# Kernel tuning notes

Hardware: AMD Instinct MI355X
Metric: run time of the kernel (lower is better)

Reference implementation:

```python
import jax, jax.numpy as jnp
import numpy as np
import math


def setup_inputs() -> dict:
    key = jax.random.key(0)
    k1, k2 = jax.random.split(key)
    q = jax.random.normal(k1, (2, 8, 2048, 64), dtype=jnp.float32)
    v = jax.random.normal(k2, (2, 8, 2048, 64), dtype=jnp.float32)
    return {"q": q, "v": v}


def reference(q, v):
    # q, v: [B, H, L, D]. Softmax-free Gaussian-kernel attention.
    # squared L2 distance via expanded form: ||qi||^2 + ||qj||^2 - 2 qi.qj
    # (same math as the original's broadcasted difference, without the
    #  O(B,H,L,L,D) intermediate)
    d = q.shape[-1]
    sq = jnp.sum(q * q, axis=-1)                      # [B, H, L]
    dots = jnp.einsum('bhid,bhjd->bhij', q, q)        # [B, H, L, L]
    sq_l2 = sq[..., :, None] + sq[..., None, :] - 2.0 * dots
    score = jnp.exp(-1.0 / (2.0 * math.sqrt(d)) * sq_l2)  # [B, H, L, L]
    return jnp.einsum('bhij,bhjd->bhid', score, v)    # [B, H, L, D]
```

## Files before the change

### kernel.cpp

```cpp
#include <hip/hip_runtime.h>
#include <hip/hip_bf16.h>
#include <stdint.h>

typedef __bf16 bf16_t;
typedef bf16_t bf16x4 __attribute__((ext_vector_type(4)));
typedef bf16_t bf16x8 __attribute__((ext_vector_type(8)));
typedef float f32x16 __attribute__((ext_vector_type(16)));
typedef float fvec4 __attribute__((ext_vector_type(4)));
typedef unsigned int u32x4v __attribute__((ext_vector_type(4)));

#define LEN 2048
#define DIM 64
#define NH  16

#define C_L8  0.18033688011112043f
#define C_L16 0.09016844005556021f

__device__ __forceinline__ float fexp2(float x) {
  float r;
  asm("v_exp_f32 %0, %1\n\ts_nop 0" : "=v"(r) : "v"(x));
  return r;
}

__device__ __forceinline__ unsigned pk2(float lo, float hi) {
  union { bf16_t h; unsigned short u; } a, b;
  a.h = (bf16_t)lo; b.h = (bf16_t)hi;
  return (unsigned)a.u | ((unsigned)b.u << 16);
}

__device__ __forceinline__ void glds16(const void* g, void* l) {
  __builtin_amdgcn_global_load_lds(
      (const __attribute__((address_space(1))) void*)g,
      (__attribute__((address_space(3))) void*)l, 16, 0, 0);
}

__device__ __forceinline__ int swk(int row, int b) {
  return row * 128 + (b ^ ((row & 7) << 4));
}
__device__ __forceinline__ int swv(int row, int b) {
  return row * 256 + (b ^ ((row & 7) << 4));
}

__global__ __launch_bounds__(256) void prepass(
    const float* __restrict__ q, const float* __restrict__ v,
    bf16_t* __restrict__ kb, bf16_t* __restrict__ vt, float* __restrict__ sqw) {
  __shared__ float wlds[64];
  const int b = blockIdx.x;
  const int h = b >> 5, jb = b & 31;
  const int t = threadIdx.x;
  const float* qh = q + ((size_t)h * LEN + jb * 64) * DIM;
  const float* vh = v + ((size_t)h * LEN + jb * 64) * DIM;

  const int dl = t & 15, jg = t >> 4;
  const int d0 = dl * 4, j0 = jg * 4;
  fvec4 r0 = *(const fvec4*)(vh + (j0 + 0) * DIM + d0);
  fvec4 r1 = *(const fvec4*)(vh + (j0 + 1) * DIM + d0);
  fvec4 r2 = *(const fvec4*)(vh + (j0 + 2) * DIM + d0);
  fvec4 r3 = *(const fvec4*)(vh + (j0 + 3) * DIM + d0);

  {
    const int j = t >> 2, kd0 = (t & 3) * 16;
    const float* qp = qh + j * DIM + kd0;
    fvec4 x0 = *(const fvec4*)(qp);
    fvec4 x1 = *(const fvec4*)(qp + 4);
    fvec4 x2 = *(const fvec4*)(qp + 8);
    fvec4 x3 = *(const fvec4*)(qp + 12);
    float s = 0.f;
    bf16x8 o0, o1;
#pragma unroll
    for (int e = 0; e < 4; ++e) {
      bf16_t h0 = (bf16_t)x0[e]; o0[e]     = h0; float f0 = (float)h0; s += f0 * f0;
      bf16_t h1 = (bf16_t)x1[e]; o0[e + 4] = h1; float f1 = (float)h1; s += f1 * f1;
      bf16_t h2 = (bf16_t)x2[e]; o1[e]     = h2; float f2 = (float)h2; s += f2 * f2;
      bf16_t h3 = (bf16_t)x3[e]; o1[e + 4] = h3; float f3 = (float)h3; s += f3 * f3;
    }
    bf16_t* kp = kb + ((size_t)h * LEN + jb * 64 + j) * DIM + kd0;
    *(bf16x8*)kp = o0;
    *(bf16x8*)(kp + 8) = o1;
    s += __shfl_xor(s, 1);
    s += __shfl_xor(s, 2);
    if ((t & 3) == 0) {
      wlds[j] = fexp2(-s * C_L16);
      sqw[h * LEN + jb * 64 + j] = s * C_L16;
    }
  }
  __syncthreads();

  {
    const float w0 = wlds[j0], w1 = wlds[j0 + 1], w2 = wlds[j0 + 2], w3 = wlds[j0 + 3];
#pragma unroll
    for (int dd = 0; dd < 4; ++dd) {
      bf16x4 o;
      o[0] = (bf16_t)(r0[dd] * w0);
      o[1] = (bf16_t)(r1[dd] * w1);
      o[2] = (bf16_t)(r2[dd] * w2);
      o[3] = (bf16_t)(r3[dd] * w3);
      *(bf16x4*)(vt + ((size_t)h * DIM + d0 + dd) * LEN + jb * 64 + j0) = o;
    }
  }
}

__global__ __launch_bounds__(512, 2) void soft_attn_main(
    const bf16_t* __restrict__ kb, const bf16_t* __restrict__ vt,
    const float* __restrict__ sqw, float* __restrict__ out) {
  __shared__ __align__(16) char smem[98304];

  const int tid  = threadIdx.x;
  const int lane = tid & 63;
  const int wave = tid >> 6;
  const int rg   = wave & 1;
  const int par  = wave >> 1;
  const int g    = lane >> 5;
  const int nn   = lane & 31;

  const int b  = blockIdx.x;
  const int wg = ((b & 7) << 5) | (b >> 3);
  const int bh = wg >> 4;
  const int qb = wg & 15;

  const bf16_t* kh  = kb + (size_t)bh * LEN * DIM;
  const bf16_t* vth = vt + (size_t)bh * DIM * LEN;

  const int qrow0 = qb * 128 + rg * 64 + nn;
  bf16x8 qf0[4], qf1[4];
  {
    const bf16_t* qp0 = kh + (size_t)qrow0 * DIM;
    const bf16_t* qp1 = kh + (size_t)(qrow0 + 32) * DIM;
#pragma unroll
    for (int kc = 0; kc < 4; ++kc) {
      qf0[kc] = *(const bf16x8*)(qp0 + kc * 16 + g * 8);
      qf1[kc] = *(const bf16x8*)(qp1 + kc * 16 + g * 8);
    }
  }
  const float hq0 = sqw[bh * LEN + qrow0];
  const float hq1 = sqw[bh * LEN + qrow0 + 32];

  const bf16_t* ksrc[2];
  const bf16_t* vsrc[2];
#pragma unroll
  for (int s = 0; s < 2; ++s) {
    const int krow = wave * 16 + s * 8 + (lane >> 3);
    const int kby  = ((lane & 7) * 16) ^ ((lane >> 3) << 4);
    ksrc[s] = kh + (size_t)krow * DIM + (kby >> 1);
    const int vrow = wave * 8 + s * 4 + (lane >> 4);
    const int vby  = ((lane & 15) * 16) ^ ((vrow & 7) << 4);
    vsrc[s] = vth + (size_t)vrow * LEN + (vby >> 1);
  }
  char* kdst = smem + wave * 2048;
  char* vdst = smem + 49152 + wave * 2048;

  f32x16 acc00 = {}, acc01 = {}, acc10 = {}, acc11 = {};

#pragma unroll
  for (int s = 0; s < 2; ++s) {
    glds16(ksrc[s], kdst + s * 1024);
    glds16(vsrc[s], vdst + s * 1024);
  }
#pragma unroll
  for (int s = 0; s < 2; ++s) {
    glds16(ksrc[s] + (size_t)128 * DIM, kdst + 16384 + s * 1024);
    glds16(vsrc[s] + (size_t)128,       vdst + 16384 + s * 1024);
  }

  int bufo = 0;
  for (int it = 0; it < 16; ++it) {
    if (it < 15) {
      asm volatile("s_waitcnt vmcnt(4)" ::: "memory");
    } else {
      asm volatile("s_waitcnt vmcnt(0)" ::: "memory");
    }
    __builtin_amdgcn_sched_barrier(0);
    __builtin_amdgcn_s_barrier();
    __builtin_amdgcn_sched_barrier(0);

    const char* kb0 = smem + bufo;
    const char* vb0 = smem + 49152 + bufo;

    bf16x8 kf0 = *(const bf16x8*)(kb0 + swk(par * 32 + nn, 0 * 32 + g * 16));
    bf16x8 kf1 = *(const bf16x8*)(kb0 + swk(par * 32 + nn, 1 * 32 + g * 16));
    bf16x8 kf2 = *(const bf16x8*)(kb0 + swk(par * 32 + nn, 2 * 32 + g * 16));
    bf16x8 kf3 = *(const bf16x8*)(kb0 + swk(par * 32 + nn, 3 * 32 + g * 16));
    f32x16 t0 = {}, t1 = {};
    __builtin_amdgcn_s_setprio(1);
    t0 = __builtin_amdgcn_mfma_f32_32x32x16_bf16(kf0, qf0[0], t0, 0, 0, 0);
    t1 = __builtin_amdgcn_mfma_f32_32x32x16_bf16(kf0, qf1[0], t1, 0, 0, 0);
    t0 = __builtin_amdgcn_mfma_f32_32x32x16_bf16(kf1, qf0[1], t0, 0, 0, 0);
    t1 = __builtin_amdgcn_mfma_f32_32x32x16_bf16(kf1, qf1[1], t1, 0, 0, 0);
    t0 = __builtin_amdgcn_mfma_f32_32x32x16_bf16(kf2, qf0[2], t0, 0, 0, 0);
    t1 = __builtin_amdgcn_mfma_f32_32x32x16_bf16(kf2, qf1[2], t1, 0, 0, 0);
    t0 = __builtin_amdgcn_mfma_f32_32x32x16_bf16(kf3, qf0[3], t0, 0, 0, 0);
    t1 = __builtin_amdgcn_mfma_f32_32x32x16_bf16(kf3, qf1[3], t1, 0, 0, 0);
    __builtin_amdgcn_s_setprio(0);

    bf16x8 af00, af01, af10, af11;
    {
      unsigned P[8];
#pragma unroll
      for (int e = 0; e < 8; ++e) {
        float s0 = fexp2(__builtin_fmaf(t0[2 * e],     C_L8, -hq0));
        float s1 = fexp2(__builtin_fmaf(t0[2 * e + 1], C_L8, -hq0));
        P[e] = pk2(s0, s1);
      }
      asm volatile("v_permlane32_swap_b32 %0, %1" : "+v"(P[0]), "+v"(P[2]));
      asm volatile("v_permlane32_swap_b32 %0, %1" : "+v"(P[1]), "+v"(P[3]));
      asm volatile("v_permlane32_swap_b32 %0, %1" : "+v"(P[4]), "+v"(P[6]));
      asm volatile("v_permlane32_swap_b32 %0, %1" : "+v"(P[5]), "+v"(P[7]));
      u32x4v f0v = { P[0], P[1], P[2], P[3] };
      u32x4v f1v = { P[4], P[5], P[6], P[7] };
      af00 = __builtin_bit_cast(bf16x8, f0v);
      af01 = __builtin_bit_cast(bf16x8, f1v);
    }
    {
      unsigned P[8];
#pragma unroll
      for (int e = 0; e < 8; ++e) {
        float s0 = fexp2(__builtin_fmaf(t1[2 * e],     C_L8, -hq1));
        float s1 = fexp2(__builtin_fmaf(t1[2 * e + 1], C_L8, -hq1));
        P[e] = pk2(s0, s1);
      }
      asm volatile("v_permlane32_swap_b32 %0, %1" : "+v"(P[0]), "+v"(P[2]));
      asm volatile("v_permlane32_swap_b32 %0, %1" : "+v"(P[1]), "+v"(P[3]));
      asm volatile("v_permlane32_swap_b32 %0, %1" : "+v"(P[4]), "+v"(P[6]));
      asm volatile("v_permlane32_swap_b32 %0, %1" : "+v"(P[5]), "+v"(P[7]));
      u32x4v f0v = { P[0], P[1], P[2], P[3] };
      u32x4v f1v = { P[4], P[5], P[6], P[7] };
      af10 = __builtin_bit_cast(bf16x8, f0v);
      af11 = __builtin_bit_cast(bf16x8, f1v);
    }

    {
      bf16x8 v0 = *(const bf16x8*)(vb0 + swv(nn,      par * 64 + g * 16));
      bf16x8 v1 = *(const bf16x8*)(vb0 + swv(32 + nn, par * 64 + g * 16));
      bf16x8 v2 = *(const bf16x8*)(vb0 + swv(nn,      par * 64 + 32 + g * 16));
      bf16x8 v3 = *(const bf16x8*)(vb0 + swv(32 + nn, par * 64 + 32 + g * 16));
      __builtin_amdgcn_s_setprio(1);
      acc00 = __builtin_amdgcn_mfma_f32_32x32x16_bf16(af00, v0, acc00, 0, 0, 0);
      acc01 = __builtin_amdgcn_mfma_f32_32x32x16_bf16(af00, v1, acc01, 0, 0, 0);
      acc10 = __builtin_amdgcn_mfma_f32_32x32x16_bf16(af10, v0, acc10, 0, 0, 0);
      acc11 = __builtin_amdgcn_mfma_f32_32x32x16_bf16(af10, v1, acc11, 0, 0, 0);
      acc00 = __builtin_amdgcn_mfma_f32_32x32x16_bf16(af01, v2, acc00, 0, 0, 0);
      acc01 = __builtin_amdgcn_mfma_f32_32x32x16_bf16(af01, v3, acc01, 0, 0, 0);
      acc10 = __builtin_amdgcn_mfma_f32_32x32x16_bf16(af11, v2, acc10, 0, 0, 0);
      acc11 = __builtin_amdgcn_mfma_f32_32x32x16_bf16(af11, v3, acc11, 0, 0, 0);
      __builtin_amdgcn_s_setprio(0);
    }

    if (it + 2 < 16) {
      int nbo = bufo + 32768; if (nbo >= 49152) nbo -= 49152;
#pragma unroll
      for (int s = 0; s < 2; ++s) {
        glds16(ksrc[s] + (size_t)(it + 2) * 128 * DIM, kdst + nbo + s * 1024);
        glds16(vsrc[s] + (size_t)(it + 2) * 128,       vdst + nbo + s * 1024);
      }
    }

    bufo += 16384; if (bufo >= 49152) bufo = 0;
  }

  __syncthreads();
  float* xb = (float*)smem;
  if (par != 0) {
    const int slot = (par - 1) * 4 + rg * 2;
    float* d0 = xb + slot * 2048;
    float* d1 = xb + (slot + 1) * 2048;
#pragma unroll
    for (int r = 0; r < 16; ++r) {
      d0[r * 64 + lane]        = acc00[r];
      d0[1024 + r * 64 + lane] = acc01[r];
      d1[r * 64 + lane]        = acc10[r];
      d1[1024 + r * 64 + lane] = acc11[r];
    }
  }
  __syncthreads();
  if (par == 0) {
    float* op = out + ((size_t)bh * LEN + qb * 128 + rg * 64) * DIM;
#pragma unroll
    for (int r = 0; r < 16; ++r) {
      const int row = (r & 3) + 8 * (r >> 2) + 4 * g;
      float a00 = acc00[r], a01 = acc01[r], a10 = acc10[r], a11 = acc11[r];
#pragma unroll
      for (int p = 1; p < 4; ++p) {
        const int slot = (p - 1) * 4 + rg * 2;
        const float* s0 = xb + slot * 2048;
        const float* s1 = xb + (slot + 1) * 2048;
        a00 += s0[r * 64 + lane];
        a01 += s0[1024 + r * 64 + lane];
        a10 += s1[r * 64 + lane];
        a11 += s1[1024 + r * 64 + lane];
      }
      op[(size_t)row * DIM + nn]               = a00;
      op[(size_t)row * DIM + 32 + nn]          = a01;
      op[(size_t)(32 + row) * DIM + nn]        = a10;
      op[(size_t)(32 + row) * DIM + 32 + nn]   = a11;
    }
  }
}

__device__ __forceinline__ int swfb(int row, int byte) {
  return row * 128 + (byte ^ ((row & 7) << 4));
}

__global__ __launch_bounds__(512, 2) void soft_attn_fb(
    const float* __restrict__ q, const float* __restrict__ v,
    float* __restrict__ out) {
  __shared__ __align__(16) char smem[33280];
  const int tid = threadIdx.x;
  const int lane = tid & 63;
  const int wave = tid >> 6;
  const int rg = wave & 3;
  const int parity = wave >> 2;
  const int tp = tid & 255;
  const int g = lane >> 5;
  const int nn = lane & 31;
  const int wg = ((blockIdx.x & 7) << 5) | (blockIdx.x >> 3);
  const int bh = wg >> 4;
  const int qb = wg & 15;
  const float* qh = q + (size_t)bh * LEN * DIM;
  const float* vh = v + (size_t)bh * LEN * DIM;
  char* kbufp = smem + parity * 8192;
  char* vbufp = smem + 16384 + parity * 8192;
  float* wkp = (float*)(smem + 32768) + parity * 64;
  const int qrow = qb * 128 + rg * 32 + nn;
  bf16x8 qf[4];
  float sq = 0.f;
  {
    const float* qp = qh + (size_t)qrow * DIM;
#pragma unroll
    for (int kc = 0; kc < 4; ++kc) {
      const int d0 = kc * 16 + g * 8;
      fvec4 x = *(const fvec4*)(qp + d0);
      fvec4 y = *(const fvec4*)(qp + d0 + 4);
      bf16x8 t;
#pragma unroll
      for (int e = 0; e < 4; ++e) {
        bf16_t h0 = (bf16_t)x[e]; t[e] = h0; float f0 = (float)h0; sq += f0 * f0;
        bf16_t h1 = (bf16_t)y[e]; t[e + 4] = h1; float f1 = (float)h1; sq += f1 * f1;
      }
      qf[kc] = t;
    }
  }
  sq += __shfl_xor(sq, 32);
  const float hq = sq * C_L16;
  f32x16 acc0 = {};
  f32x16 acc1 = {};
  for (int it = 0; it < 16; ++it) {
    const int jt = it * 2 + parity;
    const float* kg = qh + (size_t)jt * 64 * DIM;
    const float* vg = vh + (size_t)jt * 64 * DIM;
    __syncthreads();
#pragma unroll
    for (int s = 0; s < 2; ++s) {
      const int c = tp + 256 * s;
      const int j = c >> 3;
      const int d0 = (c & 7) * 8;
      fvec4 x = *(const fvec4*)(kg + j * DIM + d0);
      fvec4 y = *(const fvec4*)(kg + j * DIM + d0 + 4);
      bf16x8 t; float p = 0.f;
#pragma unroll
      for (int e = 0; e < 4; ++e) {
        bf16_t h0 = (bf16_t)x[e]; t[e] = h0; float f0 = (float)h0; p += f0 * f0;
        bf16_t h1 = (bf16_t)y[e]; t[e + 4] = h1; float f1 = (float)h1; p += f1 * f1;
      }
      *(bf16x8*)(kbufp + swfb(j, d0 * 2)) = t;
      p += __shfl_xor(p, 1);
      p += __shfl_xor(p, 2);
      p += __shfl_xor(p, 4);
      if ((lane & 7) == 0) wkp[j] = fexp2(-p * C_L16);
    }
    __syncthreads();
    float vl[2][8];
    const int vd = tp & 63;
    const int vw = tp >> 6;
#pragma unroll
    for (int s = 0; s < 2; ++s) {
      const int j0 = vw * 8 + 32 * s;
      const float* vp = vg + j0 * DIM + vd;
#pragma unroll
      for (int r = 0; r < 8; ++r) vl[s][r] = vp[r * DIM];
    }
    bf16x8 af[4];
#pragma unroll
    for (int jsub = 0; jsub < 2; ++jsub) {
      f32x16 t = {};
#pragma unroll
      for (int kc = 0; kc < 4; ++kc) {
        bf16x8 kf = *(const bf16x8*)(kbufp + swfb(jsub * 32 + nn, kc * 32 + g * 16));
        t = __builtin_amdgcn_mfma_f32_32x32x16_bf16(kf, qf[kc], t, 0, 0, 0);
      }
      unsigned P[8];
#pragma unroll
      for (int e = 0; e < 8; ++e) {
        float s0 = fexp2(__builtin_fmaf(t[2 * e], C_L8, -hq));
        float s1 = fexp2(__builtin_fmaf(t[2 * e + 1], C_L8, -hq));
        P[e] = pk2(s0, s1);
      }
      asm volatile("v_permlane32_swap_b32 %0, %1" : "+v"(P[0]), "+v"(P[2]));
      asm volatile("v_permlane32_swap_b32 %0, %1" : "+v"(P[1]), "+v"(P[3]));
      asm volatile("v_permlane32_swap_b32 %0, %1" : "+v"(P[4]), "+v"(P[6]));
      asm volatile("v_permlane32_swap_b32 %0, %1" : "+v"(P[5]), "+v"(P[7]));
      u32x4v f0v = { P[0], P[1], P[2], P[3] };
      u32x4v f1v = { P[4], P[5], P[6], P[7] };
      af[jsub * 2] = __builtin_bit_cast(bf16x8, f0v);
      af[jsub * 2 + 1] = __builtin_bit_cast(bf16x8, f1v);
    }
#pragma unroll
    for (int s = 0; s < 2; ++s) {
      const int j0 = vw * 8 + 32 * s;
      bf16x8 t;
#pragma unroll
      for (int r = 0; r < 8; ++r) {
        float w = wkp[j0 + r];
        t[r] = (bf16_t)(vl[s][r] * w);
      }
      *(bf16x8*)(vbufp + swfb(vd, j0 * 2)) = t;
    }
    __syncthreads();
#pragma unroll
    for (int kc = 0; kc < 4; ++kc) {
      bf16x8 v0 = *(const bf16x8*)(vbufp + swfb(nn, kc * 32 + g * 16));
      bf16x8 v1 = *(const bf16x8*)(vbufp + swfb(32 + nn, kc * 32 + g * 16));
      acc0 = __builtin_amdgcn_mfma_f32_32x32x16_bf16(af[kc], v0, acc0, 0, 0, 0);
      acc1 = __builtin_amdgcn_mfma_f32_32x32x16_bf16(af[kc], v1, acc1, 0, 0, 0);
    }
  }
  __syncthreads();
  float* xb = (float*)smem + rg * 2048;
  if (parity == 1) {
#pragma unroll
    for (int r = 0; r < 16; ++r) {
      xb[r * 64 + lane] = acc0[r];
      xb[(16 + r) * 64 + lane] = acc1[r];
    }
  }
  __syncthreads();
  if (parity == 0) {
    float* op = out + ((size_t)bh * LEN + qb * 128 + rg * 32) * DIM;
#pragma unroll
    for (int r = 0; r < 16; ++r) {
      const int row = (r & 3) + 8 * (r >> 2) + 4 * g;
      op[(size_t)row * DIM + nn] = acc0[r] + xb[r * 64 + lane];
      op[(size_t)row * DIM + 32 + nn] = acc1[r] + xb[(16 + r) * 64 + lane];
    }
  }
}

extern "C" void kernel_launch(void* const* d_in, const int* in_sizes, int n_in,
                              void* d_out, int out_size, void* d_ws, size_t ws_size,
                              hipStream_t stream) {
  const float* q = (const float*)d_in[0];
  const float* v = (const float*)d_in[1];
  float* out = (float*)d_out;
  (void)in_sizes; (void)n_in; (void)out_size;

  const size_t KB_BYTES = (size_t)NH * LEN * DIM * 2;
  const size_t NEED = KB_BYTES * 2 + (size_t)NH * LEN * 4;
  if (ws_size >= NEED) {
    bf16_t* kb  = (bf16_t*)d_ws;
    bf16_t* vt  = (bf16_t*)((char*)d_ws + KB_BYTES);
    float*  sqw = (float*)((char*)d_ws + KB_BYTES * 2);
    prepass<<<dim3(512), dim3(256), 0, stream>>>(q, v, kb, vt, sqw);
    soft_attn_main<<<dim3(256), dim3(512), 0, stream>>>(kb, vt, sqw, out);
  } else {
    soft_attn_fb<<<dim3(256), dim3(512), 0, stream>>>(q, v, out);
  }
}
```

Measured before the change: 96.72 us.

## Fuse bf16 prepass into main kernel via cooperative grid sync

```diff
diff --git a/kernel.cpp b/kernel.cpp
--- a/kernel.cpp
+++ b/kernel.cpp
@@ -1,6 +1,9 @@
 #include <hip/hip_runtime.h>
 #include <hip/hip_bf16.h>
+#include <hip/hip_cooperative_groups.h>
 #include <stdint.h>
+
+namespace cg = cooperative_groups;
 
 typedef __bf16 bf16_t;
 typedef bf16_t bf16x4 __attribute__((ext_vector_type(4)));
@@ -41,69 +44,12 @@
   return row * 256 + (b ^ ((row & 7) << 4));
 }
 
-__global__ __launch_bounds__(256) void prepass(
+__global__ __launch_bounds__(512, 2) void soft_attn_coop(
     const float* __restrict__ q, const float* __restrict__ v,
-    bf16_t* __restrict__ kb, bf16_t* __restrict__ vt, float* __restrict__ sqw) {
-  __shared__ float wlds[64];
-  const int b = blockIdx.x;
-  const int h = b >> 5, jb = b & 31;
-  const int t = threadIdx.x;
-  const float* qh = q + ((size_t)h * LEN + jb * 64) * DIM;
-  const float* vh = v + ((size_t)h * LEN + jb * 64) * DIM;
-
-  const int dl = t & 15, jg = t >> 4;
-  const int d0 = dl * 4, j0 = jg * 4;
-  fvec4 r0 = *(const fvec4*)(vh + (j0 + 0) * DIM + d0);
-  fvec4 r1 = *(const fvec4*)(vh + (j0 + 1) * DIM + d0);
-  fvec4 r2 = *(const fvec4*)(vh + (j0 + 2) * DIM + d0);
-  fvec4 r3 = *(const fvec4*)(vh + (j0 + 3) * DIM + d0);
-
-  {
-    const int j = t >> 2, kd0 = (t & 3) * 16;
-    const float* qp = qh + j * DIM + kd0;
-    fvec4 x0 = *(const fvec4*)(qp);
-    fvec4 x1 = *(const fvec4*)(qp + 4);
-    fvec4 x2 = *(const fvec4*)(qp + 8);
-    fvec4 x3 = *(const fvec4*)(qp + 12);
-    float s = 0.f;
-    bf16x8 o0, o1;
-#pragma unroll
-    for (int e = 0; e < 4; ++e) {
-      bf16_t h0 = (bf16_t)x0[e]; o0[e]     = h0; float f0 = (float)h0; s += f0 * f0;
-      bf16_t h1 = (bf16_t)x1[e]; o0[e + 4] = h1; float f1 = (float)h1; s += f1 * f1;
-      bf16_t h2 = (bf16_t)x2[e]; o1[e]     = h2; float f2 = (float)h2; s += f2 * f2;
-      bf16_t h3 = (bf16_t)x3[e]; o1[e + 4] = h3; float f3 = (float)h3; s += f3 * f3;
-    }
-    bf16_t* kp = kb + ((size_t)h * LEN + jb * 64 + j) * DIM + kd0;
-    *(bf16x8*)kp = o0;
-    *(bf16x8*)(kp + 8) = o1;
-    s += __shfl_xor(s, 1);
-    s += __shfl_xor(s, 2);
-    if ((t & 3) == 0) {
-      wlds[j] = fexp2(-s * C_L16);
-      sqw[h * LEN + jb * 64 + j] = s * C_L16;
-    }
-  }
-  __syncthreads();
-
-  {
-    const float w0 = wlds[j0], w1 = wlds[j0 + 1], w2 = wlds[j0 + 2], w3 = wlds[j0 + 3];
-#pragma unroll
-    for (int dd = 0; dd < 4; ++dd) {
-      bf16x4 o;
-      o[0] = (bf16_t)(r0[dd] * w0);
-      o[1] = (bf16_t)(r1[dd] * w1);
-      o[2] = (bf16_t)(r2[dd] * w2);
-      o[3] = (bf16_t)(r3[dd] * w3);
-      *(bf16x4*)(vt + ((size_t)h * DIM + d0 + dd) * LEN + jb * 64 + j0) = o;
-    }
-  }
-}
-
-__global__ __launch_bounds__(512, 2) void soft_attn_main(
-    const bf16_t* __restrict__ kb, const bf16_t* __restrict__ vt,
-    const float* __restrict__ sqw, float* __restrict__ out) {
+    bf16_t* __restrict__ kb, bf16_t* __restrict__ vt,
+    float* __restrict__ out) {
   __shared__ __align__(16) char smem[98304];
+  __shared__ float s_lds[128];
 
   const int tid  = threadIdx.x;
   const int lane = tid & 63;
@@ -118,22 +64,92 @@
   const int bh = wg >> 4;
   const int qb = wg & 15;
 
-  const bf16_t* kh  = kb + (size_t)bh * LEN * DIM;
-  const bf16_t* vth = vt + (size_t)bh * DIM * LEN;
+  const float* qh = q + (size_t)bh * LEN * DIM;
+  const float* vh = v + (size_t)bh * LEN * DIM;
+  bf16_t* khw  = kb + (size_t)bh * LEN * DIM;
+  bf16_t* vthw = vt + (size_t)bh * DIM * LEN;
+
+  const int dl = tid & 15, jg = tid >> 4;
+  const int d0 = dl * 4;
+  const int j0 = qb * 128 + jg * 4;
+  fvec4 r0 = *(const fvec4*)(vh + (size_t)(j0 + 0) * DIM + d0);
+  fvec4 r1 = *(const fvec4*)(vh + (size_t)(j0 + 1) * DIM + d0);
+  fvec4 r2 = *(const fvec4*)(vh + (size_t)(j0 + 2) * DIM + d0);
+  fvec4 r3 = *(const fvec4*)(vh + (size_t)(j0 + 3) * DIM + d0);
+
+  {
+    const int jr = tid >> 2, kd0 = (tid & 3) * 16;
+    const float* qp = qh + (size_t)(qb * 128 + jr) * DIM + kd0;
+    fvec4 x0 = *(const fvec4*)(qp);
+    fvec4 x1 = *(const fvec4*)(qp + 4);
+    fvec4 x2 = *(const fvec4*)(qp + 8);
+    fvec4 x3 = *(const fvec4*)(qp + 12);
+    float s = 0.f;
+    bf16x8 o0, o1;
+#pragma unroll
+    for (int e = 0; e < 4; ++e) {
+      bf16_t h0 = (bf16_t)x0[e]; o0[e]     = h0; float f0 = (float)h0; s += f0 * f0;
+      bf16_t h1 = (bf16_t)x1[e]; o0[e + 4] = h1; float f1 = (float)h1; s += f1 * f1;
+      bf16_t h2 = (bf16_t)x2[e]; o1[e]     = h2; float f2 = (float)h2; s += f2 * f2;
+      bf16_t h3 = (bf16_t)x3[e]; o1[e + 4] = h3; float f3 = (float)h3; s += f3 * f3;
+    }
+    bf16_t* kp = khw + (size_t)(qb * 128 + jr) * DIM + kd0;
+    *(bf16x8*)kp = o0;
+    *(bf16x8*)(kp + 8) = o1;
+    s += __shfl_xor(s, 1);
+    s += __shfl_xor(s, 2);
+    if ((tid & 3) == 0) s_lds[jr] = s * C_L16;
+  }
+  __syncthreads();
+
+  {
+    const float w0 = fexp2(-s_lds[jg * 4 + 0]);
+    const float w1 = fexp2(-s_lds[jg * 4 + 1]);
+    const float w2 = fexp2(-s_lds[jg * 4 + 2]);
+    const float w3 = fexp2(-s_lds[jg * 4 + 3]);
+#pragma unroll
+    for (int dd = 0; dd < 4; ++dd) {
+      bf16x4 o;
+      o[0] = (bf16_t)(r0[dd] * w0);
+      o[1] = (bf16_t)(r1[dd] * w1);
+      o[2] = (bf16_t)(r2[dd] * w2);
+      o[3] = (bf16_t)(r3[dd] * w3);
+      *(bf16x4*)(vthw + (size_t)(d0 + dd) * LEN + j0) = o;
+    }
+  }
 
   const int qrow0 = qb * 128 + rg * 64 + nn;
   bf16x8 qf0[4], qf1[4];
   {
-    const bf16_t* qp0 = kh + (size_t)qrow0 * DIM;
-    const bf16_t* qp1 = kh + (size_t)(qrow0 + 32) * DIM;
+    const float* qp0 = qh + (size_t)qrow0 * DIM;
+    const float* qp1 = qh + (size_t)(qrow0 + 32) * DIM;
 #pragma unroll
     for (int kc = 0; kc < 4; ++kc) {
-      qf0[kc] = *(const bf16x8*)(qp0 + kc * 16 + g * 8);
-      qf1[kc] = *(const bf16x8*)(qp1 + kc * 16 + g * 8);
-    }
-  }
-  const float hq0 = sqw[bh * LEN + qrow0];
-  const float hq1 = sqw[bh * LEN + qrow0 + 32];
+      const int dd = kc * 16 + g * 8;
+      fvec4 a0 = *(const fvec4*)(qp0 + dd);
+      fvec4 a1 = *(const fvec4*)(qp0 + dd + 4);
+      fvec4 b0 = *(const fvec4*)(qp1 + dd);
+      fvec4 b1 = *(const fvec4*)(qp1 + dd + 4);
+      bf16x8 t0v, t1v;
+#pragma unroll
+      for (int e = 0; e < 4; ++e) {
+        t0v[e]     = (bf16_t)a0[e];
+        t0v[e + 4] = (bf16_t)a1[e];
+        t1v[e]     = (bf16_t)b0[e];
+        t1v[e + 4] = (bf16_t)b1[e];
+      }
+      qf0[kc] = t0v;
+      qf1[kc] = t1v;
+    }
+  }
+  const float hq0 = s_lds[rg * 64 + nn];
+  const float hq1 = s_lds[rg * 64 + 32 + nn];
+
+  __threadfence();
+  cg::this_grid().sync();
+
+  const bf16_t* kh  = kb + (size_t)bh * LEN * DIM;
+  const bf16_t* vth = vt + (size_t)bh * DIM * LEN;
 
   const bf16_t* ksrc[2];
   const bf16_t* vsrc[2];
@@ -261,14 +277,14 @@
   float* xb = (float*)smem;
   if (par != 0) {
     const int slot = (par - 1) * 4 + rg * 2;
-    float* d0 = xb + slot * 2048;
-    float* d1 = xb + (slot + 1) * 2048;
+    float* d0p = xb + slot * 2048;
+    float* d1p = xb + (slot + 1) * 2048;
 #pragma unroll
     for (int r = 0; r < 16; ++r) {
-      d0[r * 64 + lane]        = acc00[r];
-      d0[1024 + r * 64 + lane] = acc01[r];
-      d1[r * 64 + lane]        = acc10[r];
-      d1[1024 + r * 64 + lane] = acc11[r];
+      d0p[r * 64 + lane]        = acc00[r];
+      d0p[1024 + r * 64 + lane] = acc01[r];
+      d1p[r * 64 + lane]        = acc10[r];
+      d1p[1024 + r * 64 + lane] = acc11[r];
     }
   }
   __syncthreads();
@@ -453,13 +469,13 @@
   (void)in_sizes; (void)n_in; (void)out_size;
 
   const size_t KB_BYTES = (size_t)NH * LEN * DIM * 2;
-  const size_t NEED = KB_BYTES * 2 + (size_t)NH * LEN * 4;
+  const size_t NEED = KB_BYTES * 2;
   if (ws_size >= NEED) {
-    bf16_t* kb  = (bf16_t*)d_ws;
-    bf16_t* vt  = (bf16_t*)((char*)d_ws + KB_BYTES);
-    float*  sqw = (float*)((char*)d_ws + KB_BYTES * 2);
-    prepass<<<dim3(512), dim3(256), 0, stream>>>(q, v, kb, vt, sqw);
-    soft_attn_main<<<dim3(256), dim3(512), 0, stream>>>(kb, vt, sqw, out);
+    bf16_t* kb = (bf16_t*)d_ws;
+    bf16_t* vt = (bf16_t*)((char*)d_ws + KB_BYTES);
+    void* args[] = { (void*)&q, (void*)&v, (void*)&kb, (void*)&vt, (void*)&out };
+    hipLaunchCooperativeKernel((const void*)soft_attn_coop,
+                               dim3(256), dim3(512), args, 0, stream);
   } else {
     soft_attn_fb<<<dim3(256), dim3(512), 0, stream>>>(q, v, out);
   }
```

New measurement: 179.2 us. +85.3%, slower.
